# Performance work log

Hardware: AMD Instinct MI355X
Metric: run time of the kernel (lower is better)

## Reference

```python
import jax, jax.numpy as jnp
import numpy as np

N = 10000      # nodes
E = 320000     # edges (before self-loops)
IN_DIM = 128
HID = 64
OUT = 32
HEADS = 8
NEG_SLOPE = 0.2  # PyG GATConv default leaky_relu slope


def gat_conv(x, W, a_src, a_dst, b, src, dst, num_nodes, heads, d):
    """One PyG-style GATConv layer (eval mode, concat=True).
    x: [N, F_in], W: [F_in, heads*d], a_src/a_dst: [heads, d], b: [heads*d]
    src/dst: [E'] int edge endpoints (self-loops already included).
    """
    h = (x @ W).reshape(num_nodes, heads, d)              # [N, H, D]
    alpha_s = jnp.sum(h * a_src, axis=-1)                 # [N, H]
    alpha_d = jnp.sum(h * a_dst, axis=-1)                 # [N, H]
    logits = jax.nn.leaky_relu(alpha_s[src] + alpha_d[dst], NEG_SLOPE)  # [E', H]
    # segment softmax over incoming edges of each destination node
    m = jax.lax.stop_gradient(
        jax.ops.segment_max(logits, dst, num_segments=num_nodes))      # [N, H]
    e = jnp.exp(logits - m[dst])                          # [E', H]
    denom = jax.ops.segment_sum(e, dst, num_segments=num_nodes)        # [N, H]
    alpha = e / denom[dst]                                # [E', H]
    out = jax.ops.segment_sum(alpha[:, :, None] * h[src], dst,
                              num_segments=num_nodes)     # [N, H, D]
    return out.reshape(num_nodes, heads * d) + b


def setup_inputs() -> dict:
    key = jax.random.key(0)
    ks = jax.random.split(key, 10)
    x = jax.random.normal(ks[0], (N, IN_DIM), jnp.float32)
    edge_index = jax.random.randint(ks[1], (2, E), 0, N, dtype=jnp.int64)
    s1 = 1.0 / np.sqrt(IN_DIM)
    W1 = jax.random.normal(ks[2], (IN_DIM, HEADS * HID), jnp.float32) * s1
    a1_src = jax.random.normal(ks[3], (HEADS, HID), jnp.float32) * 0.1
    a1_dst = jax.random.normal(ks[4], (HEADS, HID), jnp.float32) * 0.1
    b1 = jnp.zeros((HEADS * HID,), jnp.float32)
    s2 = 1.0 / np.sqrt(HEADS * HID)
    W2 = jax.random.normal(ks[5], (HEADS * HID, OUT), jnp.float32) * s2
    a2_src = jax.random.normal(ks[6], (1, OUT), jnp.float32) * 0.1
    a2_dst = jax.random.normal(ks[7], (1, OUT), jnp.float32) * 0.1
    b2 = jnp.zeros((OUT,), jnp.float32)
    return {"x": x, "edge_index": edge_index,
            "W1": W1, "a1_src": a1_src, "a1_dst": a1_dst, "b1": b1,
            "W2": W2, "a2_src": a2_src, "a2_dst": a2_dst, "b2": b2}


def reference(x, edge_index, W1, a1_src, a1_dst, b1, W2, a2_src, a2_dst, b2):
    # add self-loops (PyG GATConv default add_self_loops=True)
    loops = jnp.arange(N, dtype=edge_index.dtype)
    src = jnp.concatenate([edge_index[0], loops])
    dst = jnp.concatenate([edge_index[1], loops])
    # dropout layers are identity in eval mode
    h = gat_conv(x, W1, a1_src, a1_dst, b1, src, dst, N, HEADS, HID)
    h = jax.nn.elu(h)
    out = gat_conv(h, W2, a2_src, a2_dst, b2, src, dst, N, 1, OUT)
    return out
```

## Files before the change

### kernel.cpp

```cpp
#include <hip/hip_runtime.h>
#include <math.h>

#define N_NODES 10000
#define E_EDGES 320000
#define EA      (E_EDGES + N_NODES)
#define IN_DIM  128
#define HID     512
#define HEADS   8
#define OUT_DIM 32
#define NEG     0.2f
#define CAP     160
#define CAPP    164
#define N_PAD   10048
#define NRB     628
#define RB_SH   4096

#define PWB  32
#define ZBK  40
#define SCB  645

typedef __attribute__((ext_vector_type(8))) short bf16x8;
typedef __attribute__((ext_vector_type(4))) float f32x4;

__device__ __forceinline__ float leaky(float x){ return x > 0.f ? x : NEG * x; }

__device__ __forceinline__ unsigned short bf16rn(float x){
    unsigned int b = __float_as_uint(x);
    b += 0x7fffu + ((b >> 16) & 1u);
    return (unsigned short)(b >> 16);
}

__device__ __forceinline__ unsigned short f16bits(float x){
    _Float16 h = (_Float16)x;
    return __builtin_bit_cast(unsigned short, h);
}

__device__ __forceinline__ float f16val(unsigned short u){
    return (float)__builtin_bit_cast(_Float16, u);
}

__global__ void k_pre(const float* __restrict__ x, const float* __restrict__ W1,
                      int* __restrict__ cnt,
                      unsigned short* __restrict__ Ax, unsigned short* __restrict__ Bt){
    int b = blockIdx.x, t = threadIdx.x;
    if (b < NRB){
        __shared__ float xs[16 * 132];
        int rb = b;
#pragma unroll
        for (int j = 0; j < 2; j++){
            int idx = t + j * 256;
            int r = idx >> 5, c4 = idx & 31;
            int row = rb * 16 + r;
            float4 v = make_float4(0.f, 0.f, 0.f, 0.f);
            if (row < N_NODES)
                v = *reinterpret_cast<const float4*>(x + (size_t)row * IN_DIM + c4 * 4);
            *reinterpret_cast<float4*>(&xs[r * 132 + c4 * 4]) = v;
        }
        __syncthreads();
        int l15 = t & 15, kk8 = t >> 4;
        unsigned short hi[8], lo[8];
#pragma unroll
        for (int el = 0; el < 8; el++){
            float f = xs[l15 * 132 + kk8 * 8 + el];
            hi[el] = bf16rn(f);
            lo[el] = bf16rn(f - __uint_as_float((unsigned)hi[el] << 16));
        }
        uint4 H, L;
        H.x = hi[0] | ((unsigned)hi[1] << 16); H.y = hi[2] | ((unsigned)hi[3] << 16);
        H.z = hi[4] | ((unsigned)hi[5] << 16); H.w = hi[6] | ((unsigned)hi[7] << 16);
        L.x = lo[0] | ((unsigned)lo[1] << 16); L.y = lo[2] | ((unsigned)lo[3] << 16);
        L.z = lo[4] | ((unsigned)lo[5] << 16); L.w = lo[6] | ((unsigned)lo[7] << 16);
        unsigned short* base = Ax + (size_t)rb * RB_SH;
        *reinterpret_cast<uint4*>(base + (kk8 * 16 + l15) * 8) = H;
        *reinterpret_cast<uint4*>(base + 2048 + (kk8 * 16 + l15) * 8) = L;
    } else if (b < NRB + PWB){
        __shared__ float wsh[128 * 17];
        int nb = b - NRB;
        int j = t & 15, kr = t >> 4;
#pragma unroll
        for (int it = 0; it < 8; it++){
            int k = it * 16 + kr;
            wsh[k * 17 + j] = W1[(size_t)k * HID + nb * 16 + j];
        }
        __syncthreads();
        int l15 = t & 15, kk8 = t >> 4;
        unsigned short hi[8], lo[8];
#pragma unroll
        for (int el = 0; el < 8; el++){
            float f = wsh[(kk8 * 8 + el) * 17 + l15];
            hi[el] = bf16rn(f);
            lo[el] = bf16rn(f - __uint_as_float((unsigned)hi[el] << 16));
        }
        uint4 H, L;
        H.x = hi[0] | ((unsigned)hi[1] << 16); H.y = hi[2] | ((unsigned)hi[3] << 16);
        H.z = hi[4] | ((unsigned)hi[5] << 16); H.w = hi[6] | ((unsigned)hi[7] << 16);
        L.x = lo[0] | ((unsigned)lo[1] << 16); L.y = lo[2] | ((unsigned)lo[3] << 16);
        L.z = lo[4] | ((unsigned)lo[5] << 16); L.w = lo[6] | ((unsigned)lo[7] << 16);
        unsigned short* base = Bt + (size_t)nb * RB_SH;
        *reinterpret_cast<uint4*>(base + (kk8 * 16 + l15) * 8) = H;
        *reinterpret_cast<uint4*>(base + 2048 + (kk8 * 16 + l15) * 8) = L;
    } else {
        int i = (b - NRB - PWB) * 256 + t;
        if (i < N_NODES) cnt[i] = 0;
    }
}

__launch_bounds__(512)
__global__ void k_sg(const int* __restrict__ eidx, int* __restrict__ cnt,
                     int* __restrict__ esrc,
                     const unsigned short* __restrict__ Ax,
                     const unsigned short* __restrict__ Bt,
                     const float* __restrict__ a1s, const float* __restrict__ a1d,
                     unsigned short* __restrict__ h1,
                     float* __restrict__ as1, float* __restrict__ ad1){
    if (blockIdx.x < SCB){
        int e = blockIdx.x * 512 + threadIdx.x;
        if (e < EA){
            int d, s;
            if (e < E_EDGES){ s = eidx[e]; d = eidx[E_EDGES + e]; }
            else { s = d = e - E_EDGES; }
            int pos = atomicAdd(&cnt[d], 1);
            if (pos < CAP) esrc[d * CAP + pos] = s;
        }
        return;
    }
    int rb = blockIdx.x - SCB;
    int by = threadIdx.x >> 6;
    int lane = threadIdx.x & 63;
    int l15 = lane & 15, grp = lane >> 4;
    int m0 = rb * 16;
    int n0 = by * 64;
    const unsigned short* ap = Ax + (size_t)rb * RB_SH + (size_t)lane * 8;
    bf16x8 a_hi[4], a_lo[4];
#pragma unroll
    for (int ks = 0; ks < 4; ks++){
        a_hi[ks] = *reinterpret_cast<const bf16x8*>(ap + ks * 512);
        a_lo[ks] = *reinterpret_cast<const bf16x8*>(ap + 2048 + ks * 512);
    }
    const unsigned short* bp = Bt + (size_t)(by * 4) * RB_SH + (size_t)lane * 8;
    f32x4 acc[4] = {};
#pragma unroll
    for (int ks = 0; ks < 4; ks++){
#pragma unroll
        for (int ns = 0; ns < 4; ns++){
            const unsigned short* bb = bp + (size_t)ns * RB_SH + ks * 512;
            bf16x8 b_hi = *reinterpret_cast<const bf16x8*>(bb);
            bf16x8 b_lo = *reinterpret_cast<const bf16x8*>(bb + 2048);
            acc[ns] = __builtin_amdgcn_mfma_f32_16x16x32_bf16(a_hi[ks], b_hi, acc[ns], 0, 0, 0);
            acc[ns] = __builtin_amdgcn_mfma_f32_16x16x32_bf16(a_lo[ks], b_hi, acc[ns], 0, 0, 0);
            acc[ns] = __builtin_amdgcn_mfma_f32_16x16x32_bf16(a_hi[ks], b_lo, acc[ns], 0, 0, 0);
        }
    }
    float vs[4] = {0.f, 0.f, 0.f, 0.f}, vd[4] = {0.f, 0.f, 0.f, 0.f};
#pragma unroll
    for (int ns = 0; ns < 4; ns++){
        int c = n0 + ns * 16 + l15;
        float a_s = a1s[c], a_d = a1d[c];
#pragma unroll
        for (int r = 0; r < 4; r++){
            float v = acc[ns][r];
            int rr = m0 + grp * 4 + r;
            if (rr < N_NODES) h1[(size_t)rr * HID + c] = f16bits(v);
            vs[r] += v * a_s; vd[r] += v * a_d;
        }
    }
#pragma unroll
    for (int r = 0; r < 4; r++){
#pragma unroll
        for (int off = 8; off >= 1; off >>= 1){
            vs[r] += __shfl_xor(vs[r], off);
            vd[r] += __shfl_xor(vd[r], off);
        }
    }
    if (l15 == 0){
#pragma unroll
        for (int r = 0; r < 4; r++){
            int rr = m0 + grp * 4 + r;
            if (rr < N_NODES){ as1[rr * HEADS + by] = vs[r]; ad1[rr * HEADS + by] = vd[r]; }
        }
    }
}

__launch_bounds__(128)
__global__ void k_agg1(const unsigned short* __restrict__ h1,
                       const float* __restrict__ as1, const float* __restrict__ ad1,
                       const int* __restrict__ cnt, const int* __restrict__ esrc,
                       const float* __restrict__ b1, float* __restrict__ h1b){
    int gp = blockIdx.x & 3;
    int ng = blockIdx.x >> 2;
    int t  = threadIdx.x;
    int sub = t >> 4;
    int tl  = t & 15;
    int n = ng * 8 + sub;
    int g0 = gp * 2, g1 = g0 + 1;
    int c = cnt[n]; if (c > CAP) c = CAP;
    int beg = n * CAP;
    __shared__ float s_w0[8][CAPP];
    __shared__ float s_w1[8][CAPP];
    __shared__ unsigned s_off[8][CAPP];
    float adn0 = ad1[(n << 3) + g0];
    float adn1 = ad1[(n << 3) + g1];
    float pm0 = -INFINITY, pm1 = -INFINITY;
    for (int i = tl; i < c; i += 16){
        int s = esrc[beg + i];
        float lg0 = leaky(as1[(s << 3) + g0] + adn0);
        float lg1 = leaky(as1[(s << 3) + g1] + adn1);
        s_w0[sub][i] = lg0; s_w1[sub][i] = lg1;
        s_off[sub][i] = (unsigned)s << 9;
        pm0 = fmaxf(pm0, lg0); pm1 = fmaxf(pm1, lg1);
    }
#pragma unroll
    for (int off = 8; off >= 1; off >>= 1){
        pm0 = fmaxf(pm0, __shfl_xor(pm0, off, 16));
        pm1 = fmaxf(pm1, __shfl_xor(pm1, off, 16));
    }
    __syncthreads();
    for (int i = tl; i < c; i += 16){
        s_w0[sub][i] = __expf(s_w0[sub][i] - pm0);
        s_w1[sub][i] = __expf(s_w1[sub][i] - pm1);
    }
    __syncthreads();
    unsigned dbase = (unsigned)(gp * 128 + tl * 8);
    const float* swp = (tl >= 8) ? &s_w1[sub][0] : &s_w0[sub][0];
    const unsigned* sop = &s_off[sub][0];
    float ac[4][8] = {};
    float dn[4] = {};
    int i = 0;
    for (; i + 3 < c; i += 4){
#pragma unroll
        for (int u = 0; u < 4; u++){
            float w = swp[i + u];
            uint4 hv = *reinterpret_cast<const uint4*>(h1 + sop[i + u] + dbase);
            ac[u][0] += w * f16val((unsigned short)(hv.x & 0xffffu));
            ac[u][1] += w * f16val((unsigned short)(hv.x >> 16));
            ac[u][2] += w * f16val((unsigned short)(hv.y & 0xffffu));
            ac[u][3] += w * f16val((unsigned short)(hv.y >> 16));
            ac[u][4] += w * f16val((unsigned short)(hv.z & 0xffffu));
            ac[u][5] += w * f16val((unsigned short)(hv.z >> 16));
            ac[u][6] += w * f16val((unsigned short)(hv.w & 0xffffu));
            ac[u][7] += w * f16val((unsigned short)(hv.w >> 16));
            dn[u] += w;
        }
    }
    for (; i < c; i++){
        float w = swp[i];
        uint4 hv = *reinterpret_cast<const uint4*>(h1 + sop[i] + dbase);
        ac[0][0] += w * f16val((unsigned short)(hv.x & 0xffffu));
        ac[0][1] += w * f16val((unsigned short)(hv.x >> 16));
        ac[0][2] += w * f16val((unsigned short)(hv.y & 0xffffu));
        ac[0][3] += w * f16val((unsigned short)(hv.y >> 16));
        ac[0][4] += w * f16val((unsigned short)(hv.z & 0xffffu));
        ac[0][5] += w * f16val((unsigned short)(hv.z >> 16));
        ac[0][6] += w * f16val((unsigned short)(hv.w & 0xffffu));
        ac[0][7] += w * f16val((unsigned short)(hv.w >> 16));
        dn[0] += w;
    }
    float den = (dn[0] + dn[1]) + (dn[2] + dn[3]);
    float rd = 1.f / den;
    float4 bv0 = *reinterpret_cast<const float4*>(b1 + dbase);
    float4 bv1 = *reinterpret_cast<const float4*>(b1 + dbase + 4);
    float o[8];
#pragma unroll
    for (int j = 0; j < 8; j++){
        float v = ((ac[0][j] + ac[1][j]) + (ac[2][j] + ac[3][j])) * rd;
        float bb = (j < 4) ? (&bv0.x)[j] : (&bv1.x)[j - 4];
        v += bb;
        o[j] = v > 0.f ? v : expm1f(v);
    }
    float4 o0, o1;
    o0.x = o[0]; o0.y = o[1]; o0.z = o[2]; o0.w = o[3];
    o1.x = o[4]; o1.y = o[5]; o1.z = o[6]; o1.w = o[7];
    *reinterpret_cast<float4*>(h1b + (size_t)n * HID + dbase) = o0;
    *reinterpret_cast<float4*>(h1b + (size_t)n * HID + dbase + 4) = o1;
}

__launch_bounds__(128)
__global__ void k_gemm2(const float* __restrict__ h1b, const float* __restrict__ W2,
                        const float* __restrict__ a2s, const float* __restrict__ a2d,
                        float* __restrict__ h2, float* __restrict__ as2,
                        float* __restrict__ ad2){
    __shared__ float hs[16 * 516];
    int t = threadIdx.x;
    int n0 = blockIdx.x * 16;
    const float4* src = reinterpret_cast<const float4*>(h1b + (size_t)n0 * HID);
    for (int i = t; i < 2048; i += 128){
        int r = i >> 7, c4 = i & 127;
        *reinterpret_cast<float4*>(&hs[r * 516 + c4 * 4]) = src[i];
    }
    __syncthreads();
    int nl = t >> 3, cg = t & 7, c0 = cg * 4;
    float a0 = 0.f, a1 = 0.f, a2 = 0.f, a3 = 0.f;
#pragma unroll 2
    for (int k4 = 0; k4 < 128; k4++){
        float4 hv = *reinterpret_cast<const float4*>(&hs[nl * 516 + k4 * 4]);
        float4 w0 = *reinterpret_cast<const float4*>(W2 + (k4 * 4 + 0) * OUT_DIM + c0);
        float4 w1 = *reinterpret_cast<const float4*>(W2 + (k4 * 4 + 1) * OUT_DIM + c0);
        float4 w2 = *reinterpret_cast<const float4*>(W2 + (k4 * 4 + 2) * OUT_DIM + c0);
        float4 w3 = *reinterpret_cast<const float4*>(W2 + (k4 * 4 + 3) * OUT_DIM + c0);
        a0 += hv.x * w0.x + hv.y * w1.x + hv.z * w2.x + hv.w * w3.x;
        a1 += hv.x * w0.y + hv.y * w1.y + hv.z * w2.y + hv.w * w3.y;
        a2 += hv.x * w0.z + hv.y * w1.z + hv.z * w2.z + hv.w * w3.z;
        a3 += hv.x * w0.w + hv.y * w1.w + hv.z * w2.w + hv.w * w3.w;
    }
    float4 o; o.x = a0; o.y = a1; o.z = a2; o.w = a3;
    *reinterpret_cast<float4*>(h2 + (size_t)(n0 + nl) * OUT_DIM + c0) = o;
    float4 s4 = *reinterpret_cast<const float4*>(a2s + c0);
    float4 d4 = *reinterpret_cast<const float4*>(a2d + c0);
    float vs = a0 * s4.x + a1 * s4.y + a2 * s4.z + a3 * s4.w;
    float vd = a0 * d4.x + a1 * d4.y + a2 * d4.z + a3 * d4.w;
#pragma unroll
    for (int off = 4; off >= 1; off >>= 1){
        vs += __shfl_xor(vs, off);
        vd += __shfl_xor(vd, off);
    }
    if (cg == 0){ as2[n0 + nl] = vs; ad2[n0 + nl] = vd; }
}

__launch_bounds__(256)
__global__ void k_agg2(const float* __restrict__ h2, const float* __restrict__ as2,
                       const float* __restrict__ ad2, const int* __restrict__ cnt,
                       const int* __restrict__ esrc,
                       const float* __restrict__ b2, float* __restrict__ out){
    int wv = threadIdx.x >> 6;
    int lane = threadIdx.x & 63;
    int n = blockIdx.x * 4 + wv;
    __shared__ float    s_w[4][CAPP];
    __shared__ unsigned s_off[4][CAPP];
    int c = cnt[n]; if (c > CAP) c = CAP;
    int beg = n * CAP;
    float adn = ad2[n];
    float pm = -INFINITY;
    for (int i = lane; i < c; i += 64){
        int s = esrc[beg + i];
        float lg = leaky(as2[s] + adn);
        s_off[wv][i] = (unsigned)s * OUT_DIM;
        s_w[wv][i] = lg;
        pm = fmaxf(pm, lg);
    }
#pragma unroll
    for (int off = 32; off >= 1; off >>= 1)
        pm = fmaxf(pm, __shfl_xor(pm, off));
    __syncthreads();
    for (int i = lane; i < c; i += 64) s_w[wv][i] = __expf(s_w[wv][i] - pm);
    __syncthreads();
    int eslot = lane >> 3, dgrp = lane & 7, d0 = dgrp * 4;
    float4 acc = make_float4(0.f, 0.f, 0.f, 0.f);
    float den = 0.f;
    for (int i = eslot; i < c; i += 8){
        float w = s_w[wv][i];
        float4 hv = *reinterpret_cast<const float4*>(h2 + s_off[wv][i] + d0);
        acc.x += w * hv.x; acc.y += w * hv.y;
        acc.z += w * hv.z; acc.w += w * hv.w;
        den += w;
    }
#pragma unroll
    for (int off = 8; off <= 32; off <<= 1){
        acc.x += __shfl_xor(acc.x, off);
        acc.y += __shfl_xor(acc.y, off);
        acc.z += __shfl_xor(acc.z, off);
        acc.w += __shfl_xor(acc.w, off);
        den   += __shfl_xor(den, off);
    }
    if (eslot == 0){
        float rd = 1.f / den;
        float4 bv = *reinterpret_cast<const float4*>(b2 + d0);
        float4 o;
        o.x = acc.x * rd + bv.x; o.y = acc.y * rd + bv.y;
        o.z = acc.z * rd + bv.z; o.w = acc.w * rd + bv.w;
        *reinterpret_cast<float4*>(out + (size_t)n * OUT_DIM + d0) = o;
    }
}

extern "C" void kernel_launch(void* const* d_in, const int* in_sizes, int n_in,
                              void* d_out, int out_size, void* d_ws, size_t ws_size,
                              hipStream_t stream){
    const float* x   = (const float*)d_in[0];
    const int*  eidx = (const int*)  d_in[1];
    const float* W1  = (const float*)d_in[2];
    const float* a1s = (const float*)d_in[3];
    const float* a1d = (const float*)d_in[4];
    const float* b1  = (const float*)d_in[5];
    const float* W2  = (const float*)d_in[6];
    const float* a2s = (const float*)d_in[7];
    const float* a2d = (const float*)d_in[8];
    const float* b2  = (const float*)d_in[9];
    float* out = (float*)d_out;

    char* ws = (char*)d_ws;
    size_t off = 0;
    auto alloc = [&](size_t bytes) -> void* {
        void* p = ws + off;
        off += (bytes + 255) & ~(size_t)255;
        return p;
    };
    unsigned short* h1 = (unsigned short*)alloc((size_t)N_NODES * HID * 2);
    float* h1b  = (float*)alloc((size_t)N_NODES * HID * 4);
    unsigned short* Bt = (unsigned short*)alloc((size_t)32 * RB_SH * 2);
    float* as1  = (float*)alloc((size_t)N_NODES * HEADS * 4);
    float* ad1  = (float*)alloc((size_t)N_NODES * HEADS * 4);
    float* h2   = (float*)alloc((size_t)N_NODES * OUT_DIM * 4);
    float* vs2  = (float*)alloc((size_t)N_NODES * 4);
    float* vd2  = (float*)alloc((size_t)N_NODES * 4);
    int* cnt    = (int*)alloc((size_t)N_NODES * 4);
    int* esrc   = (int*)alloc((size_t)N_NODES * CAP * 4);
    unsigned short* Ax = (unsigned short*)h1b;

    k_pre <<<NRB + PWB + ZBK, 256, 0, stream>>>(x, W1, cnt, Ax, Bt);
    k_sg  <<<SCB + NRB, 512, 0, stream>>>(eidx, cnt, esrc, Ax, Bt, a1s, a1d,
                                          h1, as1, ad1);
    k_agg1<<<(N_NODES / 8) * 4, 128, 0, stream>>>(h1, as1, ad1, cnt, esrc, b1, h1b);
    k_gemm2<<<N_NODES / 16, 128, 0, stream>>>(h1b, W2, a2s, a2d, h2, vs2, vd2);
    k_agg2<<<N_NODES / 4, 256, 0, stream>>>(h2, vs2, vd2, cnt, esrc, b2, out);
}
```

Before: 109.5 us.

## Fuse all GAT stages into one cooperative persistent kernel with grid syncs

Replaces the five separate kernel launches (preprocess, scatter+GEMM1, aggregate1, GEMM2, aggregate2) with a single cooperative kernel. Its grid is sized from occupancy and capped at 512 blocks, and the stages are separated by grid.sync(). Each stage loops over its work units persistently, and GEMM2 now uses 32-row tiles with two output columns per thread. The aim is to remove launch overhead and inter-kernel gaps. In exchange, grid-wide barriers and reduced parallelism per stage may leave CUs idle during load-imbalanced phases.

```diff
diff --git a/kernel.cpp b/kernel.cpp
--- a/kernel.cpp
+++ b/kernel.cpp
@@ -1,5 +1,8 @@
 #include <hip/hip_runtime.h>
+#include <hip/hip_cooperative_groups.h>
 #include <math.h>
+
+namespace cg = cooperative_groups;
 
 #define N_NODES 10000
 #define E_EDGES 320000
@@ -11,13 +14,8 @@
 #define NEG     0.2f
 #define CAP     160
 #define CAPP    164
-#define N_PAD   10048
 #define NRB     628
 #define RB_SH   4096
-
-#define PWB  32
-#define ZBK  40
-#define SCB  645
 
 typedef __attribute__((ext_vector_type(8))) short bf16x8;
 typedef __attribute__((ext_vector_type(4))) float f32x4;
@@ -39,335 +37,382 @@
     return (float)__builtin_bit_cast(_Float16, u);
 }
 
-__global__ void k_pre(const float* __restrict__ x, const float* __restrict__ W1,
-                      int* __restrict__ cnt,
-                      unsigned short* __restrict__ Ax, unsigned short* __restrict__ Bt){
-    int b = blockIdx.x, t = threadIdx.x;
-    if (b < NRB){
-        __shared__ float xs[16 * 132];
-        int rb = b;
-#pragma unroll
-        for (int j = 0; j < 2; j++){
-            int idx = t + j * 256;
-            int r = idx >> 5, c4 = idx & 31;
-            int row = rb * 16 + r;
-            float4 v = make_float4(0.f, 0.f, 0.f, 0.f);
-            if (row < N_NODES)
-                v = *reinterpret_cast<const float4*>(x + (size_t)row * IN_DIM + c4 * 4);
-            *reinterpret_cast<float4*>(&xs[r * 132 + c4 * 4]) = v;
+__global__ __launch_bounds__(512, 4) void k_fused(
+    const float* __restrict__ x, const int* __restrict__ eidx,
+    const float* __restrict__ W1,
+    const float* __restrict__ a1s, const float* __restrict__ a1d,
+    const float* __restrict__ b1,
+    const float* __restrict__ W2, const float* __restrict__ a2s,
+    const float* __restrict__ a2d, const float* __restrict__ b2,
+    float* __restrict__ out,
+    unsigned short* __restrict__ h1, float* __restrict__ h1b,
+    unsigned short* __restrict__ Ax, unsigned short* __restrict__ Bt,
+    float* __restrict__ as1, float* __restrict__ ad1,
+    float* __restrict__ h2, float* __restrict__ vs2, float* __restrict__ vd2,
+    int* __restrict__ cnt, int* __restrict__ esrc)
+{
+    cg::grid_group grid = cg::this_grid();
+    __shared__ __align__(16) char smem[66048];
+    const int t = threadIdx.x;
+    const int b = blockIdx.x;
+    const int G = gridDim.x;
+
+    for (int i = b * 512 + t; i < N_NODES; i += G * 512) cnt[i] = 0;
+    {
+        int half = t >> 8, tt = t & 255;
+        float* xs = reinterpret_cast<float*>(smem) + half * (16 * 132);
+        const int NIT0 = (NRB + 2 * G - 1) / (2 * G);
+        for (int it = 0; it < NIT0; it++){
+            int u = it * 2 * G + b * 2 + half;
+            bool act = (u < NRB);
+#pragma unroll
+            for (int j = 0; j < 2; j++){
+                int idx = tt + j * 256;
+                int r = idx >> 5, c4 = idx & 31;
+                int row = u * 16 + r;
+                float4 v = make_float4(0.f, 0.f, 0.f, 0.f);
+                if (act && row < N_NODES)
+                    v = *reinterpret_cast<const float4*>(x + (size_t)row * IN_DIM + c4 * 4);
+                if (act) *reinterpret_cast<float4*>(&xs[r * 132 + c4 * 4]) = v;
+            }
+            __syncthreads();
+            if (act){
+                int l15 = tt & 15, kk8 = tt >> 4;
+                unsigned short hi[8], lo[8];
+#pragma unroll
+                for (int el = 0; el < 8; el++){
+                    float f = xs[l15 * 132 + kk8 * 8 + el];
+                    hi[el] = bf16rn(f);
+                    lo[el] = bf16rn(f - __uint_as_float((unsigned)hi[el] << 16));
+                }
+                uint4 H, L;
+                H.x = hi[0] | ((unsigned)hi[1] << 16); H.y = hi[2] | ((unsigned)hi[3] << 16);
+                H.z = hi[4] | ((unsigned)hi[5] << 16); H.w = hi[6] | ((unsigned)hi[7] << 16);
+                L.x = lo[0] | ((unsigned)lo[1] << 16); L.y = lo[2] | ((unsigned)lo[3] << 16);
+                L.z = lo[4] | ((unsigned)lo[5] << 16); L.w = lo[6] | ((unsigned)lo[7] << 16);
+                unsigned short* base = Ax + (size_t)u * RB_SH;
+                *reinterpret_cast<uint4*>(base + (kk8 * 16 + l15) * 8) = H;
+                *reinterpret_cast<uint4*>(base + 2048 + (kk8 * 16 + l15) * 8) = L;
+            }
+            __syncthreads();
+        }
+    }
+    {
+        int half = t >> 8, tt = t & 255;
+        float* wsh = reinterpret_cast<float*>(smem) + half * (128 * 17);
+        int u = b * 2 + half;
+        bool act = (u < 32);
+        int j = tt & 15, kr = tt >> 4;
+        if (act){
+#pragma unroll
+            for (int it = 0; it < 8; it++){
+                int k = it * 16 + kr;
+                wsh[k * 17 + j] = W1[(size_t)k * HID + u * 16 + j];
+            }
         }
         __syncthreads();
-        int l15 = t & 15, kk8 = t >> 4;
-        unsigned short hi[8], lo[8];
-#pragma unroll
-        for (int el = 0; el < 8; el++){
-            float f = xs[l15 * 132 + kk8 * 8 + el];
-            hi[el] = bf16rn(f);
-            lo[el] = bf16rn(f - __uint_as_float((unsigned)hi[el] << 16));
-        }
-        uint4 H, L;
-        H.x = hi[0] | ((unsigned)hi[1] << 16); H.y = hi[2] | ((unsigned)hi[3] << 16);
-        H.z = hi[4] | ((unsigned)hi[5] << 16); H.w = hi[6] | ((unsigned)hi[7] << 16);
-        L.x = lo[0] | ((unsigned)lo[1] << 16); L.y = lo[2] | ((unsigned)lo[3] << 16);
-        L.z = lo[4] | ((unsigned)lo[5] << 16); L.w = lo[6] | ((unsigned)lo[7] << 16);
-        unsigned short* base = Ax + (size_t)rb * RB_SH;
-        *reinterpret_cast<uint4*>(base + (kk8 * 16 + l15) * 8) = H;
-        *reinterpret_cast<uint4*>(base + 2048 + (kk8 * 16 + l15) * 8) = L;
-    } else if (b < NRB + PWB){
-        __shared__ float wsh[128 * 17];
-        int nb = b - NRB;
-        int j = t & 15, kr = t >> 4;
-#pragma unroll
-        for (int it = 0; it < 8; it++){
-            int k = it * 16 + kr;
-            wsh[k * 17 + j] = W1[(size_t)k * HID + nb * 16 + j];
+        if (act){
+            int l15 = tt & 15, kk8 = tt >> 4;
+            unsigned short hi[8], lo[8];
+#pragma unroll
+            for (int el = 0; el < 8; el++){
+                float f = wsh[(kk8 * 8 + el) * 17 + l15];
+                hi[el] = bf16rn(f);
+                lo[el] = bf16rn(f - __uint_as_float((unsigned)hi[el] << 16));
+            }
+            uint4 H, L;
+            H.x = hi[0] | ((unsigned)hi[1] << 16); H.y = hi[2] | ((unsigned)hi[3] << 16);
+            H.z = hi[4] | ((unsigned)hi[5] << 16); H.w = hi[6] | ((unsigned)hi[7] << 16);
+            L.x = lo[0] | ((unsigned)lo[1] << 16); L.y = lo[2] | ((unsigned)lo[3] << 16);
+            L.z = lo[4] | ((unsigned)lo[5] << 16); L.w = lo[6] | ((unsigned)lo[7] << 16);
+            unsigned short* base = Bt + (size_t)u * RB_SH;
+            *reinterpret_cast<uint4*>(base + (kk8 * 16 + l15) * 8) = H;
+            *reinterpret_cast<uint4*>(base + 2048 + (kk8 * 16 + l15) * 8) = L;
         }
         __syncthreads();
-        int l15 = t & 15, kk8 = t >> 4;
-        unsigned short hi[8], lo[8];
-#pragma unroll
-        for (int el = 0; el < 8; el++){
-            float f = wsh[(kk8 * 8 + el) * 17 + l15];
-            hi[el] = bf16rn(f);
-            lo[el] = bf16rn(f - __uint_as_float((unsigned)hi[el] << 16));
-        }
-        uint4 H, L;
-        H.x = hi[0] | ((unsigned)hi[1] << 16); H.y = hi[2] | ((unsigned)hi[3] << 16);
-        H.z = hi[4] | ((unsigned)hi[5] << 16); H.w = hi[6] | ((unsigned)hi[7] << 16);
-        L.x = lo[0] | ((unsigned)lo[1] << 16); L.y = lo[2] | ((unsigned)lo[3] << 16);
-        L.z = lo[4] | ((unsigned)lo[5] << 16); L.w = lo[6] | ((unsigned)lo[7] << 16);
-        unsigned short* base = Bt + (size_t)nb * RB_SH;
-        *reinterpret_cast<uint4*>(base + (kk8 * 16 + l15) * 8) = H;
-        *reinterpret_cast<uint4*>(base + 2048 + (kk8 * 16 + l15) * 8) = L;
-    } else {
-        int i = (b - NRB - PWB) * 256 + t;
-        if (i < N_NODES) cnt[i] = 0;
-    }
-}
-
-__launch_bounds__(512)
-__global__ void k_sg(const int* __restrict__ eidx, int* __restrict__ cnt,
-                     int* __restrict__ esrc,
-                     const unsigned short* __restrict__ Ax,
-                     const unsigned short* __restrict__ Bt,
-                     const float* __restrict__ a1s, const float* __restrict__ a1d,
-                     unsigned short* __restrict__ h1,
-                     float* __restrict__ as1, float* __restrict__ ad1){
-    if (blockIdx.x < SCB){
-        int e = blockIdx.x * 512 + threadIdx.x;
-        if (e < EA){
-            int d, s;
-            if (e < E_EDGES){ s = eidx[e]; d = eidx[E_EDGES + e]; }
-            else { s = d = e - E_EDGES; }
-            int pos = atomicAdd(&cnt[d], 1);
-            if (pos < CAP) esrc[d * CAP + pos] = s;
-        }
-        return;
-    }
-    int rb = blockIdx.x - SCB;
-    int by = threadIdx.x >> 6;
-    int lane = threadIdx.x & 63;
-    int l15 = lane & 15, grp = lane >> 4;
-    int m0 = rb * 16;
-    int n0 = by * 64;
-    const unsigned short* ap = Ax + (size_t)rb * RB_SH + (size_t)lane * 8;
-    bf16x8 a_hi[4], a_lo[4];
-#pragma unroll
-    for (int ks = 0; ks < 4; ks++){
-        a_hi[ks] = *reinterpret_cast<const bf16x8*>(ap + ks * 512);
-        a_lo[ks] = *reinterpret_cast<const bf16x8*>(ap + 2048 + ks * 512);
-    }
-    const unsigned short* bp = Bt + (size_t)(by * 4) * RB_SH + (size_t)lane * 8;
-    f32x4 acc[4] = {};
-#pragma unroll
-    for (int ks = 0; ks < 4; ks++){
-#pragma unroll
-        for (int ns = 0; ns < 4; ns++){
-            const unsigned short* bb = bp + (size_t)ns * RB_SH + ks * 512;
-            bf16x8 b_hi = *reinterpret_cast<const bf16x8*>(bb);
-            bf16x8 b_lo = *reinterpret_cast<const bf16x8*>(bb + 2048);
-            acc[ns] = __builtin_amdgcn_mfma_f32_16x16x32_bf16(a_hi[ks], b_hi, acc[ns], 0, 0, 0);
-            acc[ns] = __builtin_amdgcn_mfma_f32_16x16x32_bf16(a_lo[ks], b_hi, acc[ns], 0, 0, 0);
-            acc[ns] = __builtin_amdgcn_mfma_f32_16x16x32_bf16(a_hi[ks], b_lo, acc[ns], 0, 0, 0);
-        }
-    }
-    float vs[4] = {0.f, 0.f, 0.f, 0.f}, vd[4] = {0.f, 0.f, 0.f, 0.f};
-#pragma unroll
-    for (int ns = 0; ns < 4; ns++){
-        int c = n0 + ns * 16 + l15;
-        float a_s = a1s[c], a_d = a1d[c];
-#pragma unroll
-        for (int r = 0; r < 4; r++){
-            float v = acc[ns][r];
-            int rr = m0 + grp * 4 + r;
-            if (rr < N_NODES) h1[(size_t)rr * HID + c] = f16bits(v);
-            vs[r] += v * a_s; vd[r] += v * a_d;
-        }
-    }
-#pragma unroll
-    for (int r = 0; r < 4; r++){
-#pragma unroll
-        for (int off = 8; off >= 1; off >>= 1){
-            vs[r] += __shfl_xor(vs[r], off);
-            vd[r] += __shfl_xor(vd[r], off);
-        }
-    }
-    if (l15 == 0){
-#pragma unroll
-        for (int r = 0; r < 4; r++){
-            int rr = m0 + grp * 4 + r;
-            if (rr < N_NODES){ as1[rr * HEADS + by] = vs[r]; ad1[rr * HEADS + by] = vd[r]; }
-        }
-    }
-}
-
-__launch_bounds__(128)
-__global__ void k_agg1(const unsigned short* __restrict__ h1,
-                       const float* __restrict__ as1, const float* __restrict__ ad1,
-                       const int* __restrict__ cnt, const int* __restrict__ esrc,
-                       const float* __restrict__ b1, float* __restrict__ h1b){
-    int gp = blockIdx.x & 3;
-    int ng = blockIdx.x >> 2;
-    int t  = threadIdx.x;
-    int sub = t >> 4;
-    int tl  = t & 15;
-    int n = ng * 8 + sub;
-    int g0 = gp * 2, g1 = g0 + 1;
-    int c = cnt[n]; if (c > CAP) c = CAP;
-    int beg = n * CAP;
-    __shared__ float s_w0[8][CAPP];
-    __shared__ float s_w1[8][CAPP];
-    __shared__ unsigned s_off[8][CAPP];
-    float adn0 = ad1[(n << 3) + g0];
-    float adn1 = ad1[(n << 3) + g1];
-    float pm0 = -INFINITY, pm1 = -INFINITY;
-    for (int i = tl; i < c; i += 16){
-        int s = esrc[beg + i];
-        float lg0 = leaky(as1[(s << 3) + g0] + adn0);
-        float lg1 = leaky(as1[(s << 3) + g1] + adn1);
-        s_w0[sub][i] = lg0; s_w1[sub][i] = lg1;
-        s_off[sub][i] = (unsigned)s << 9;
-        pm0 = fmaxf(pm0, lg0); pm1 = fmaxf(pm1, lg1);
-    }
-#pragma unroll
-    for (int off = 8; off >= 1; off >>= 1){
-        pm0 = fmaxf(pm0, __shfl_xor(pm0, off, 16));
-        pm1 = fmaxf(pm1, __shfl_xor(pm1, off, 16));
-    }
-    __syncthreads();
-    for (int i = tl; i < c; i += 16){
-        s_w0[sub][i] = __expf(s_w0[sub][i] - pm0);
-        s_w1[sub][i] = __expf(s_w1[sub][i] - pm1);
-    }
-    __syncthreads();
-    unsigned dbase = (unsigned)(gp * 128 + tl * 8);
-    const float* swp = (tl >= 8) ? &s_w1[sub][0] : &s_w0[sub][0];
-    const unsigned* sop = &s_off[sub][0];
-    float ac[4][8] = {};
-    float dn[4] = {};
-    int i = 0;
-    for (; i + 3 < c; i += 4){
-#pragma unroll
-        for (int u = 0; u < 4; u++){
-            float w = swp[i + u];
-            uint4 hv = *reinterpret_cast<const uint4*>(h1 + sop[i + u] + dbase);
-            ac[u][0] += w * f16val((unsigned short)(hv.x & 0xffffu));
-            ac[u][1] += w * f16val((unsigned short)(hv.x >> 16));
-            ac[u][2] += w * f16val((unsigned short)(hv.y & 0xffffu));
-            ac[u][3] += w * f16val((unsigned short)(hv.y >> 16));
-            ac[u][4] += w * f16val((unsigned short)(hv.z & 0xffffu));
-            ac[u][5] += w * f16val((unsigned short)(hv.z >> 16));
-            ac[u][6] += w * f16val((unsigned short)(hv.w & 0xffffu));
-            ac[u][7] += w * f16val((unsigned short)(hv.w >> 16));
-            dn[u] += w;
-        }
-    }
-    for (; i < c; i++){
-        float w = swp[i];
-        uint4 hv = *reinterpret_cast<const uint4*>(h1 + sop[i] + dbase);
-        ac[0][0] += w * f16val((unsigned short)(hv.x & 0xffffu));
-        ac[0][1] += w * f16val((unsigned short)(hv.x >> 16));
-        ac[0][2] += w * f16val((unsigned short)(hv.y & 0xffffu));
-        ac[0][3] += w * f16val((unsigned short)(hv.y >> 16));
-        ac[0][4] += w * f16val((unsigned short)(hv.z & 0xffffu));
-        ac[0][5] += w * f16val((unsigned short)(hv.z >> 16));
-        ac[0][6] += w * f16val((unsigned short)(hv.w & 0xffffu));
-        ac[0][7] += w * f16val((unsigned short)(hv.w >> 16));
-        dn[0] += w;
-    }
-    float den = (dn[0] + dn[1]) + (dn[2] + dn[3]);
-    float rd = 1.f / den;
-    float4 bv0 = *reinterpret_cast<const float4*>(b1 + dbase);
-    float4 bv1 = *reinterpret_cast<const float4*>(b1 + dbase + 4);
-    float o[8];
-#pragma unroll
-    for (int j = 0; j < 8; j++){
-        float v = ((ac[0][j] + ac[1][j]) + (ac[2][j] + ac[3][j])) * rd;
-        float bb = (j < 4) ? (&bv0.x)[j] : (&bv1.x)[j - 4];
-        v += bb;
-        o[j] = v > 0.f ? v : expm1f(v);
-    }
-    float4 o0, o1;
-    o0.x = o[0]; o0.y = o[1]; o0.z = o[2]; o0.w = o[3];
-    o1.x = o[4]; o1.y = o[5]; o1.z = o[6]; o1.w = o[7];
-    *reinterpret_cast<float4*>(h1b + (size_t)n * HID + dbase) = o0;
-    *reinterpret_cast<float4*>(h1b + (size_t)n * HID + dbase + 4) = o1;
-}
-
-__launch_bounds__(128)
-__global__ void k_gemm2(const float* __restrict__ h1b, const float* __restrict__ W2,
-                        const float* __restrict__ a2s, const float* __restrict__ a2d,
-                        float* __restrict__ h2, float* __restrict__ as2,
-                        float* __restrict__ ad2){
-    __shared__ float hs[16 * 516];
-    int t = threadIdx.x;
-    int n0 = blockIdx.x * 16;
-    const float4* src = reinterpret_cast<const float4*>(h1b + (size_t)n0 * HID);
-    for (int i = t; i < 2048; i += 128){
-        int r = i >> 7, c4 = i & 127;
-        *reinterpret_cast<float4*>(&hs[r * 516 + c4 * 4]) = src[i];
-    }
-    __syncthreads();
-    int nl = t >> 3, cg = t & 7, c0 = cg * 4;
-    float a0 = 0.f, a1 = 0.f, a2 = 0.f, a3 = 0.f;
-#pragma unroll 2
-    for (int k4 = 0; k4 < 128; k4++){
-        float4 hv = *reinterpret_cast<const float4*>(&hs[nl * 516 + k4 * 4]);
-        float4 w0 = *reinterpret_cast<const float4*>(W2 + (k4 * 4 + 0) * OUT_DIM + c0);
-        float4 w1 = *reinterpret_cast<const float4*>(W2 + (k4 * 4 + 1) * OUT_DIM + c0);
-        float4 w2 = *reinterpret_cast<const float4*>(W2 + (k4 * 4 + 2) * OUT_DIM + c0);
-        float4 w3 = *reinterpret_cast<const float4*>(W2 + (k4 * 4 + 3) * OUT_DIM + c0);
-        a0 += hv.x * w0.x + hv.y * w1.x + hv.z * w2.x + hv.w * w3.x;
-        a1 += hv.x * w0.y + hv.y * w1.y + hv.z * w2.y + hv.w * w3.y;
-        a2 += hv.x * w0.z + hv.y * w1.z + hv.z * w2.z + hv.w * w3.z;
-        a3 += hv.x * w0.w + hv.y * w1.w + hv.z * w2.w + hv.w * w3.w;
-    }
-    float4 o; o.x = a0; o.y = a1; o.z = a2; o.w = a3;
-    *reinterpret_cast<float4*>(h2 + (size_t)(n0 + nl) * OUT_DIM + c0) = o;
-    float4 s4 = *reinterpret_cast<const float4*>(a2s + c0);
-    float4 d4 = *reinterpret_cast<const float4*>(a2d + c0);
-    float vs = a0 * s4.x + a1 * s4.y + a2 * s4.z + a3 * s4.w;
-    float vd = a0 * d4.x + a1 * d4.y + a2 * d4.z + a3 * d4.w;
-#pragma unroll
-    for (int off = 4; off >= 1; off >>= 1){
-        vs += __shfl_xor(vs, off);
-        vd += __shfl_xor(vd, off);
-    }
-    if (cg == 0){ as2[n0 + nl] = vs; ad2[n0 + nl] = vd; }
-}
-
-__launch_bounds__(256)
-__global__ void k_agg2(const float* __restrict__ h2, const float* __restrict__ as2,
-                       const float* __restrict__ ad2, const int* __restrict__ cnt,
-                       const int* __restrict__ esrc,
-                       const float* __restrict__ b2, float* __restrict__ out){
-    int wv = threadIdx.x >> 6;
-    int lane = threadIdx.x & 63;
-    int n = blockIdx.x * 4 + wv;
-    __shared__ float    s_w[4][CAPP];
-    __shared__ unsigned s_off[4][CAPP];
-    int c = cnt[n]; if (c > CAP) c = CAP;
-    int beg = n * CAP;
-    float adn = ad2[n];
-    float pm = -INFINITY;
-    for (int i = lane; i < c; i += 64){
-        int s = esrc[beg + i];
-        float lg = leaky(as2[s] + adn);
-        s_off[wv][i] = (unsigned)s * OUT_DIM;
-        s_w[wv][i] = lg;
-        pm = fmaxf(pm, lg);
-    }
-#pragma unroll
-    for (int off = 32; off >= 1; off >>= 1)
-        pm = fmaxf(pm, __shfl_xor(pm, off));
-    __syncthreads();
-    for (int i = lane; i < c; i += 64) s_w[wv][i] = __expf(s_w[wv][i] - pm);
-    __syncthreads();
-    int eslot = lane >> 3, dgrp = lane & 7, d0 = dgrp * 4;
-    float4 acc = make_float4(0.f, 0.f, 0.f, 0.f);
-    float den = 0.f;
-    for (int i = eslot; i < c; i += 8){
-        float w = s_w[wv][i];
-        float4 hv = *reinterpret_cast<const float4*>(h2 + s_off[wv][i] + d0);
-        acc.x += w * hv.x; acc.y += w * hv.y;
-        acc.z += w * hv.z; acc.w += w * hv.w;
-        den += w;
-    }
-#pragma unroll
-    for (int off = 8; off <= 32; off <<= 1){
-        acc.x += __shfl_xor(acc.x, off);
-        acc.y += __shfl_xor(acc.y, off);
-        acc.z += __shfl_xor(acc.z, off);
-        acc.w += __shfl_xor(acc.w, off);
-        den   += __shfl_xor(den, off);
-    }
-    if (eslot == 0){
-        float rd = 1.f / den;
-        float4 bv = *reinterpret_cast<const float4*>(b2 + d0);
-        float4 o;
-        o.x = acc.x * rd + bv.x; o.y = acc.y * rd + bv.y;
-        o.z = acc.z * rd + bv.z; o.w = acc.w * rd + bv.w;
-        *reinterpret_cast<float4*>(out + (size_t)n * OUT_DIM + d0) = o;
+    }
+    grid.sync();
+
+    for (int e = b * 512 + t; e < EA; e += G * 512){
+        int d, s;
+        if (e < E_EDGES){ s = eidx[e]; d = eidx[E_EDGES + e]; }
+        else { s = d = e - E_EDGES; }
+        int pos = atomicAdd(&cnt[d], 1);
+        if (pos < CAP) esrc[d * CAP + pos] = s;
+    }
+    {
+        int by = t >> 6;
+        int lane = t & 63;
+        int l15 = lane & 15, grp = lane >> 4;
+        for (int u = b; u < NRB; u += G){
+            int m0 = u * 16;
+            int n0 = by * 64;
+            const unsigned short* ap = Ax + (size_t)u * RB_SH + (size_t)lane * 8;
+            bf16x8 a_hi[4], a_lo[4];
+#pragma unroll
+            for (int ks = 0; ks < 4; ks++){
+                a_hi[ks] = *reinterpret_cast<const bf16x8*>(ap + ks * 512);
+                a_lo[ks] = *reinterpret_cast<const bf16x8*>(ap + 2048 + ks * 512);
+            }
+            const unsigned short* bp = Bt + (size_t)(by * 4) * RB_SH + (size_t)lane * 8;
+            f32x4 acc[4] = {};
+#pragma unroll
+            for (int ks = 0; ks < 4; ks++){
+#pragma unroll
+                for (int ns = 0; ns < 4; ns++){
+                    const unsigned short* bb = bp + (size_t)ns * RB_SH + ks * 512;
+                    bf16x8 b_hi = *reinterpret_cast<const bf16x8*>(bb);
+                    bf16x8 b_lo = *reinterpret_cast<const bf16x8*>(bb + 2048);
+                    acc[ns] = __builtin_amdgcn_mfma_f32_16x16x32_bf16(a_hi[ks], b_hi, acc[ns], 0, 0, 0);
+                    acc[ns] = __builtin_amdgcn_mfma_f32_16x16x32_bf16(a_lo[ks], b_hi, acc[ns], 0, 0, 0);
+                    acc[ns] = __builtin_amdgcn_mfma_f32_16x16x32_bf16(a_hi[ks], b_lo, acc[ns], 0, 0, 0);
+                }
+            }
+            float vs[4] = {0.f, 0.f, 0.f, 0.f}, vd[4] = {0.f, 0.f, 0.f, 0.f};
+#pragma unroll
+            for (int ns = 0; ns < 4; ns++){
+                int c = n0 + ns * 16 + l15;
+                float a_s = a1s[c], a_d = a1d[c];
+#pragma unroll
+                for (int r = 0; r < 4; r++){
+                    float v = acc[ns][r];
+                    int rr = m0 + grp * 4 + r;
+                    if (rr < N_NODES) h1[(size_t)rr * HID + c] = f16bits(v);
+                    vs[r] += v * a_s; vd[r] += v * a_d;
+                }
+            }
+#pragma unroll
+            for (int r = 0; r < 4; r++){
+#pragma unroll
+                for (int off = 8; off >= 1; off >>= 1){
+                    vs[r] += __shfl_xor(vs[r], off);
+                    vd[r] += __shfl_xor(vd[r], off);
+                }
+            }
+            if (l15 == 0){
+#pragma unroll
+                for (int r = 0; r < 4; r++){
+                    int rr = m0 + grp * 4 + r;
+                    if (rr < N_NODES){ as1[rr * HEADS + by] = vs[r]; ad1[rr * HEADS + by] = vd[r]; }
+                }
+            }
+        }
+    }
+    grid.sync();
+
+    {
+        int gp = b & 3;
+        int sub128 = t >> 7;
+        int tt = t & 127;
+        int sub = tt >> 4;
+        int tl = tt & 15;
+        int lrow = sub128 * 8 + sub;
+        int g0 = gp * 2, g1 = g0 + 1;
+        float* s_w0 = reinterpret_cast<float*>(smem);
+        float* s_w1 = s_w0 + 32 * CAPP;
+        unsigned* s_off = reinterpret_cast<unsigned*>(s_w1 + 32 * CAPP);
+        const int NIT = (1250 + G - 1) / G;
+        for (int it = 0; it < NIT; it++){
+            int u = it * G + (b >> 2) * 4 + sub128;
+            bool act = (u < 1250);
+            int n = act ? (u * 8 + sub) : 0;
+            int c = 0, beg = 0;
+            float adn0 = 0.f, adn1 = 0.f;
+            if (act){
+                c = cnt[n]; if (c > CAP) c = CAP;
+                beg = n * CAP;
+                adn0 = ad1[(n << 3) + g0];
+                adn1 = ad1[(n << 3) + g1];
+            }
+            float pm0 = -INFINITY, pm1 = -INFINITY;
+            for (int i = tl; i < c; i += 16){
+                int s = esrc[beg + i];
+                float lg0 = leaky(as1[(s << 3) + g0] + adn0);
+                float lg1 = leaky(as1[(s << 3) + g1] + adn1);
+                s_w0[lrow * CAPP + i] = lg0;
+                s_w1[lrow * CAPP + i] = lg1;
+                s_off[lrow * CAPP + i] = (unsigned)s << 9;
+                pm0 = fmaxf(pm0, lg0); pm1 = fmaxf(pm1, lg1);
+            }
+#pragma unroll
+            for (int off = 8; off >= 1; off >>= 1){
+                pm0 = fmaxf(pm0, __shfl_xor(pm0, off, 16));
+                pm1 = fmaxf(pm1, __shfl_xor(pm1, off, 16));
+            }
+            __syncthreads();
+            for (int i = tl; i < c; i += 16){
+                s_w0[lrow * CAPP + i] = __expf(s_w0[lrow * CAPP + i] - pm0);
+                s_w1[lrow * CAPP + i] = __expf(s_w1[lrow * CAPP + i] - pm1);
+            }
+            __syncthreads();
+            unsigned dbase = (unsigned)(gp * 128 + tl * 8);
+            const float* swp = (tl >= 8) ? &s_w1[lrow * CAPP] : &s_w0[lrow * CAPP];
+            const unsigned* sop = &s_off[lrow * CAPP];
+            float ac[4][8] = {};
+            float dn[4] = {};
+            int i = 0;
+            for (; i + 3 < c; i += 4){
+#pragma unroll
+                for (int uu = 0; uu < 4; uu++){
+                    float w = swp[i + uu];
+                    uint4 hv = *reinterpret_cast<const uint4*>(h1 + sop[i + uu] + dbase);
+                    ac[uu][0] += w * f16val((unsigned short)(hv.x & 0xffffu));
+                    ac[uu][1] += w * f16val((unsigned short)(hv.x >> 16));
+                    ac[uu][2] += w * f16val((unsigned short)(hv.y & 0xffffu));
+                    ac[uu][3] += w * f16val((unsigned short)(hv.y >> 16));
+                    ac[uu][4] += w * f16val((unsigned short)(hv.z & 0xffffu));
+                    ac[uu][5] += w * f16val((unsigned short)(hv.z >> 16));
+                    ac[uu][6] += w * f16val((unsigned short)(hv.w & 0xffffu));
+                    ac[uu][7] += w * f16val((unsigned short)(hv.w >> 16));
+                    dn[uu] += w;
+                }
+            }
+            for (; i < c; i++){
+                float w = swp[i];
+                uint4 hv = *reinterpret_cast<const uint4*>(h1 + sop[i] + dbase);
+                ac[0][0] += w * f16val((unsigned short)(hv.x & 0xffffu));
+                ac[0][1] += w * f16val((unsigned short)(hv.x >> 16));
+                ac[0][2] += w * f16val((unsigned short)(hv.y & 0xffffu));
+                ac[0][3] += w * f16val((unsigned short)(hv.y >> 16));
+                ac[0][4] += w * f16val((unsigned short)(hv.z & 0xffffu));
+                ac[0][5] += w * f16val((unsigned short)(hv.z >> 16));
+                ac[0][6] += w * f16val((unsigned short)(hv.w & 0xffffu));
+                ac[0][7] += w * f16val((unsigned short)(hv.w >> 16));
+                dn[0] += w;
+            }
+            if (act){
+                float den = (dn[0] + dn[1]) + (dn[2] + dn[3]);
+                float rd = 1.f / den;
+                float4 bv0 = *reinterpret_cast<const float4*>(b1 + dbase);
+                float4 bv1 = *reinterpret_cast<const float4*>(b1 + dbase + 4);
+                float o[8];
+#pragma unroll
+                for (int j = 0; j < 8; j++){
+                    float v = ((ac[0][j] + ac[1][j]) + (ac[2][j] + ac[3][j])) * rd;
+                    float bb = (j < 4) ? (&bv0.x)[j] : (&bv1.x)[j - 4];
+                    v += bb;
+                    o[j] = v > 0.f ? v : expm1f(v);
+                }
+                float4 o0, o1;
+                o0.x = o[0]; o0.y = o[1]; o0.z = o[2]; o0.w = o[3];
+                o1.x = o[4]; o1.y = o[5]; o1.z = o[6]; o1.w = o[7];
+                *reinterpret_cast<float4*>(h1b + (size_t)n * HID + dbase) = o0;
+                *reinterpret_cast<float4*>(h1b + (size_t)n * HID + dbase + 4) = o1;
+            }
+            __syncthreads();
+        }
+    }
+    grid.sync();
+
+    {
+        float* hs = reinterpret_cast<float*>(smem);
+        const int NU = (N_NODES + 31) / 32;
+        const int NIT3 = (NU + G - 1) / G;
+        int nl = t >> 4, cg = t & 15, c0 = cg * 2;
+        for (int it = 0; it < NIT3; it++){
+            int u = it * G + b;
+            bool act = (u < NU);
+            for (int i = t; i < 4096; i += 512){
+                int r = i >> 7, c4 = i & 127;
+                int row = u * 32 + r;
+                float4 v = make_float4(0.f, 0.f, 0.f, 0.f);
+                if (act && row < N_NODES)
+                    v = *reinterpret_cast<const float4*>(h1b + (size_t)row * HID + c4 * 4);
+                if (act) *reinterpret_cast<float4*>(&hs[r * 516 + c4 * 4]) = v;
+            }
+            __syncthreads();
+            float a0 = 0.f, a1 = 0.f;
+#pragma unroll 4
+            for (int k4 = 0; k4 < 128; k4++){
+                float4 hv = *reinterpret_cast<const float4*>(&hs[nl * 516 + k4 * 4]);
+                const float* wp = W2 + (size_t)(k4 * 4) * OUT_DIM + c0;
+                float2 w0 = *reinterpret_cast<const float2*>(wp);
+                float2 w1 = *reinterpret_cast<const float2*>(wp + OUT_DIM);
+                float2 w2 = *reinterpret_cast<const float2*>(wp + 2 * OUT_DIM);
+                float2 w3 = *reinterpret_cast<const float2*>(wp + 3 * OUT_DIM);
+                a0 += hv.x * w0.x + hv.y * w1.x + hv.z * w2.x + hv.w * w3.x;
+                a1 += hv.x * w0.y + hv.y * w1.y + hv.z * w2.y + hv.w * w3.y;
+            }
+            int row = u * 32 + nl;
+            bool rowok = act && (row < N_NODES);
+            if (rowok){
+                float2 o; o.x = a0; o.y = a1;
+                *reinterpret_cast<float2*>(h2 + (size_t)row * OUT_DIM + c0) = o;
+            }
+            float vs = a0 * a2s[c0] + a1 * a2s[c0 + 1];
+            float vd = a0 * a2d[c0] + a1 * a2d[c0 + 1];
+#pragma unroll
+            for (int off = 8; off >= 1; off >>= 1){
+                vs += __shfl_xor(vs, off, 16);
+                vd += __shfl_xor(vd, off, 16);
+            }
+            if (cg == 0 && rowok){ vs2[row] = vs; vd2[row] = vd; }
+            __syncthreads();
+        }
+    }
+    grid.sync();
+
+    {
+        int half = t >> 8, tt = t & 255;
+        int wv = tt >> 6, lane = tt & 63;
+        int lrow = half * 4 + wv;
+        float* s_w = reinterpret_cast<float*>(smem);
+        unsigned* s_off = reinterpret_cast<unsigned*>(s_w + 8 * CAPP);
+        const int NIT4 = (2500 + 2 * G - 1) / (2 * G);
+        for (int it = 0; it < NIT4; it++){
+            int u = it * 2 * G + b * 2 + half;
+            bool act = (u < 2500);
+            int n = act ? (u * 4 + wv) : 0;
+            int c = 0, beg = 0;
+            float adn = 0.f;
+            if (act){
+                c = cnt[n]; if (c > CAP) c = CAP;
+                beg = n * CAP;
+                adn = vd2[n];
+            }
+            float pm = -INFINITY;
+            for (int i = lane; i < c; i += 64){
+                int s = esrc[beg + i];
+                float lg = leaky(vs2[s] + adn);
+                s_off[lrow * CAPP + i] = (unsigned)s * OUT_DIM;
+                s_w[lrow * CAPP + i] = lg;
+                pm = fmaxf(pm, lg);
+            }
+#pragma unroll
+            for (int off = 32; off >= 1; off >>= 1)
+                pm = fmaxf(pm, __shfl_xor(pm, off));
+            __syncthreads();
+            for (int i = lane; i < c; i += 64)
+                s_w[lrow * CAPP + i] = __expf(s_w[lrow * CAPP + i] - pm);
+            __syncthreads();
+            int eslot = lane >> 3, dgrp = lane & 7, d0 = dgrp * 4;
+            float4 acc = make_float4(0.f, 0.f, 0.f, 0.f);
+            float den = 0.f;
+            for (int i = eslot; i < c; i += 8){
+                float w = s_w[lrow * CAPP + i];
+                float4 hv = *reinterpret_cast<const float4*>(h2 + s_off[lrow * CAPP + i] + d0);
+                acc.x += w * hv.x; acc.y += w * hv.y;
+                acc.z += w * hv.z; acc.w += w * hv.w;
+                den += w;
+            }
+#pragma unroll
+            for (int off = 8; off <= 32; off <<= 1){
+                acc.x += __shfl_xor(acc.x, off);
+                acc.y += __shfl_xor(acc.y, off);
+                acc.z += __shfl_xor(acc.z, off);
+                acc.w += __shfl_xor(acc.w, off);
+                den   += __shfl_xor(den, off);
+            }
+            if (eslot == 0 && act){
+                float rd = 1.f / den;
+                float4 bv = *reinterpret_cast<const float4*>(b2 + d0);
+                float4 o;
+                o.x = acc.x * rd + bv.x; o.y = acc.y * rd + bv.y;
+                o.z = acc.z * rd + bv.z; o.w = acc.w * rd + bv.w;
+                *reinterpret_cast<float4*>(out + (size_t)n * OUT_DIM + d0) = o;
+            }
+            __syncthreads();
+        }
     }
 }
 
@@ -405,10 +450,20 @@
     int* esrc   = (int*)alloc((size_t)N_NODES * CAP * 4);
     unsigned short* Ax = (unsigned short*)h1b;
 
-    k_pre <<<NRB + PWB + ZBK, 256, 0, stream>>>(x, W1, cnt, Ax, Bt);
-    k_sg  <<<SCB + NRB, 512, 0, stream>>>(eidx, cnt, esrc, Ax, Bt, a1s, a1d,
-                                          h1, as1, ad1);
-    k_agg1<<<(N_NODES / 8) * 4, 128, 0, stream>>>(h1, as1, ad1, cnt, esrc, b1, h1b);
-    k_gemm2<<<N_NODES / 16, 128, 0, stream>>>(h1b, W2, a2s, a2d, h2, vs2, vd2);
-    k_agg2<<<N_NODES / 4, 256, 0, stream>>>(h2, vs2, vd2, cnt, esrc, b2, out);
+    int maxb = 0;
+    hipOccupancyMaxActiveBlocksPerMultiprocessor(&maxb, (const void*)k_fused, 512, 0);
+    if (maxb < 1) maxb = 1;
+    long grid = (long)maxb * 256;
+    if (grid > 512) grid = 512;
+    grid &= ~3L;
+    if (grid < 4) grid = 4;
+
+    void* args[] = {
+        (void*)&x, (void*)&eidx, (void*)&W1, (void*)&a1s, (void*)&a1d, (void*)&b1,
+        (void*)&W2, (void*)&a2s, (void*)&a2d, (void*)&b2, (void*)&out,
+        (void*)&h1, (void*)&h1b, (void*)&Ax, (void*)&Bt, (void*)&as1, (void*)&ad1,
+        (void*)&h2, (void*)&vs2, (void*)&vd2, (void*)&cnt, (void*)&esrc
+    };
+    hipLaunchCooperativeKernel((const void*)k_fused, dim3((int)grid), dim3(512),
+                               args, 0, stream);
 }
```

Result: slower. 308.4 us (+181.6%).
